# Kernel tuning notes

Hardware: AMD Instinct MI355X
Metric: run time of the kernel (lower is better)

Reference implementation:

```python
import jax, jax.numpy as jnp
import numpy as np

H = 64  # hidden size (fixed by module)

def _gru_cell(x, h, Wih, Whh, bih, bhh):
    # PyTorch GRU cell: gates ordered (r, z, n)
    gi = x @ Wih.T + bih            # [B, 3H]
    gh = h @ Whh.T + bhh            # [B, 3H]
    ir, iz, inn = jnp.split(gi, 3, axis=-1)
    hr, hz, hn = jnp.split(gh, 3, axis=-1)
    r = jax.nn.sigmoid(ir + hr)
    z = jax.nn.sigmoid(iz + hz)
    n = jnp.tanh(inn + r * hn)
    return (1.0 - z) * n + z * h


def setup_inputs() -> dict:
    key = jax.random.key(0)
    ks = jax.random.split(key, 24)
    B, T, NI = 16384, 256, 6
    s = 1.0 / np.sqrt(H)  # torch default GRU init scale
    f32 = jnp.float32
    u = lambda k, shp: jax.random.uniform(k, shp, dtype=f32, minval=-s, maxval=s)
    inp = {
        "x": jax.random.normal(ks[0], (B, T, NI), dtype=f32),
        "target_len": 180,
        # encoder GRU, layer 0 (input size NI) and layer 1 (input size H)
        "e_Wih0": u(ks[1], (3 * H, NI)), "e_Whh0": u(ks[2], (3 * H, H)),
        "e_bih0": u(ks[3], (3 * H,)),    "e_bhh0": u(ks[4], (3 * H,)),
        "e_Wih1": u(ks[5], (3 * H, H)),  "e_Whh1": u(ks[6], (3 * H, H)),
        "e_bih1": u(ks[7], (3 * H,)),    "e_bhh1": u(ks[8], (3 * H,)),
        # decoder GRU, layer 0 (input size 1) and layer 1 (input size H)
        "d_Wih0": u(ks[9], (3 * H, 1)),  "d_Whh0": u(ks[10], (3 * H, H)),
        "d_bih0": u(ks[11], (3 * H,)),   "d_bhh0": u(ks[12], (3 * H,)),
        "d_Wih1": u(ks[13], (3 * H, H)), "d_Whh1": u(ks[14], (3 * H, H)),
        "d_bih1": u(ks[15], (3 * H,)),   "d_bhh1": u(ks[16], (3 * H,)),
        # heads
        "W_on": u(ks[17], (1, H)), "b_on": u(ks[18], (1,)),
        "W_cv": u(ks[19], (1, H)), "b_cv": u(ks[20], (1,)),
    }
    return inp


def reference(x, target_len,
              e_Wih0, e_Whh0, e_bih0, e_bhh0, e_Wih1, e_Whh1, e_bih1, e_bhh1,
              d_Wih0, d_Whh0, d_bih0, d_bhh0, d_Wih1, d_Whh1, d_bih1, d_bhh1,
              W_on, b_on, W_cv, b_cv):
    B = x.shape[0]
    on_threshold = 0.5

    # ---- encoder: 2-layer GRU over the input sequence, keep final hidden ----
    def enc_step(carry, xt):
        h0, h1 = carry
        h0 = _gru_cell(xt, h0, e_Wih0, e_Whh0, e_bih0, e_bhh0)
        h1 = _gru_cell(h0, h1, e_Wih1, e_Whh1, e_bih1, e_bhh1)
        return (h0, h1), None

    h_init = (jnp.zeros((B, H), x.dtype), jnp.zeros((B, H), x.dtype))
    (h0, h1), _ = jax.lax.scan(enc_step, h_init, jnp.swapaxes(x, 0, 1))  # [T,B,NI]

    def dec_step(carry, _):
        prev, h0, h1 = carry                                   # prev: [B,1]
        h0 = _gru_cell(prev, h0, d_Wih0, d_Whh0, d_bih0, d_bhh0)
        h1 = _gru_cell(h0, h1, d_Wih1, d_Whh1, d_bih1, d_bhh1)
        cv = h1 @ W_cv.T + b_cv                                # [B,1]
        logit = h1 @ W_on.T + b_on                             # [B,1]
        gated = (jax.nn.sigmoid(logit) > on_threshold).astype(cv.dtype) * cv
        return (gated, h0, h1), gated

    prev0 = jnp.zeros((B, 1), x.dtype)
    _, outs = jax.lax.scan(dec_step, (prev0, h0, h1), None, length=target_len)
    # outs: [target_len, B, 1] -> [B, target_len, 1] (torch.cat along dim=1)
    return jnp.swapaxes(outs, 0, 1)
```

## Files before the change

### kernel.cpp

```cpp
#include <hip/hip_runtime.h>
#include <math.h>

#define TENC 256
#define NIE  6
#define LH   68
#define WSTR 68

__shared__ float sW1[192 * WSTR];
__shared__ float sU1[192 * WSTR];
__shared__ float sHd[132];
__shared__ float shs[3][64 * LH];

__device__ __forceinline__ float sigm_(float x) {
    return __builtin_amdgcn_rcpf(1.0f + __expf(-x));
}
__device__ __forceinline__ float tanh_(float x) {
    float t = __expf(2.0f * x);
    return (t - 1.0f) * __builtin_amdgcn_rcpf(t + 1.0f);
}

__device__ __forceinline__ void fma4(float& acc, const float4& a, const float4& b) {
    acc = fmaf(a.x, b.x, acc);
    acc = fmaf(a.y, b.y, acc);
    acc = fmaf(a.z, b.z, acc);
    acc = fmaf(a.w, b.w, acc);
}

__device__ __forceinline__ void stage_w1(const float* __restrict__ W1,
                                         const float* __restrict__ U1) {
    for (int s = threadIdx.x; s < 12288; s += 512) {
        int k = s & 63, row = s >> 6;
        int g = row >> 6, j = row & 63;
        int d = (j * 3 + g) * WSTR + k;
        sW1[d] = W1[s];
        sU1[d] = U1[s];
    }
}

template<int KIN>
__device__ __forceinline__ void layer0_c(const float* __restrict__ U0,
                                         const float* w0r, const float* w0z,
                                         const float* w0n,
                                         const float* xin,
                                         const float* b_r, const float* b_z,
                                         const float* b_nx, const float* b_nh,
                                         int jB, int bl,
                                         const float* __restrict__ hb,
                                         float hn[2][4])
{
    float ar[2][4], az[2][4], anx[2][4], anh[2][4];
#pragma unroll
    for (int g = 0; g < 4; ++g) {
#pragma unroll
        for (int jj = 0; jj < 2; ++jj) {
            ar[jj][g] = b_r[jj]; az[jj][g] = b_z[jj];
            anx[jj][g] = b_nx[jj]; anh[jj][g] = b_nh[jj];
        }
    }
#pragma unroll
    for (int jj = 0; jj < 2; ++jj)
#pragma unroll
        for (int g = 0; g < 4; ++g)
#pragma unroll
            for (int k = 0; k < KIN; ++k) {
                ar[jj][g]  = fmaf(w0r[jj * KIN + k], xin[g * KIN + k], ar[jj][g]);
                az[jj][g]  = fmaf(w0z[jj * KIN + k], xin[g * KIN + k], az[jj][g]);
                anx[jj][g] = fmaf(w0n[jj * KIN + k], xin[g * KIN + k], anx[jj][g]);
            }
    const float* u0 = U0 + (size_t)jB * 64;
    const float* u1 = U0 + (size_t)(jB + 1) * 64;
    const float* hr0 = hb + bl * LH;
#pragma unroll 2
    for (int kc = 0; kc < 64; kc += 4) {
        float4 hv[4];
#pragma unroll
        for (int g = 0; g < 4; ++g)
            hv[g] = *(const float4*)(hr0 + g * (16 * LH) + kc);
        float4 r0 = *(const float4*)(u0 + kc);
        float4 z0 = *(const float4*)(u0 + 4096 + kc);
        float4 n0 = *(const float4*)(u0 + 8192 + kc);
        float4 r1 = *(const float4*)(u1 + kc);
        float4 z1 = *(const float4*)(u1 + 4096 + kc);
        float4 n1 = *(const float4*)(u1 + 8192 + kc);
#pragma unroll
        for (int g = 0; g < 4; ++g) {
            fma4(ar[0][g], r0, hv[g]); fma4(az[0][g], z0, hv[g]); fma4(anh[0][g], n0, hv[g]);
            fma4(ar[1][g], r1, hv[g]); fma4(az[1][g], z1, hv[g]); fma4(anh[1][g], n1, hv[g]);
        }
    }
#pragma unroll
    for (int g = 0; g < 4; ++g) {
        float2 ho = *(const float2*)(hb + (bl + 16 * g) * LH + jB);
        float hold[2] = {ho.x, ho.y};
#pragma unroll
        for (int jj = 0; jj < 2; ++jj) {
            float r = sigm_(ar[jj][g]);
            float z = sigm_(az[jj][g]);
            float n = tanh_(fmaf(r, anh[jj][g], anx[jj][g]));
            hn[jj][g] = fmaf(z, hold[jj] - n, n);
        }
    }
}

__device__ __forceinline__ void layer1_c(const float* b_r, const float* b_z,
                                         const float* b_nx, const float* b_nh,
                                         int jB, int bl,
                                         const float* __restrict__ xb,
                                         const float* __restrict__ hb,
                                         float hn[2][4])
{
    float ar[2][4], az[2][4], anx[2][4], anh[2][4];
#pragma unroll
    for (int g = 0; g < 4; ++g) {
#pragma unroll
        for (int jj = 0; jj < 2; ++jj) {
            ar[jj][g] = b_r[jj]; az[jj][g] = b_z[jj];
            anx[jj][g] = b_nx[jj]; anh[jj][g] = b_nh[jj];
        }
    }
    const float* wb0 = sW1 + (jB * 3) * WSTR;
    const float* wb1 = sW1 + ((jB + 1) * 3) * WSTR;
    const float* ub0 = sU1 + (jB * 3) * WSTR;
    const float* ub1 = sU1 + ((jB + 1) * 3) * WSTR;
    const float* xr0 = xb + bl * LH;
    const float* hr0 = hb + bl * LH;
#pragma unroll 2
    for (int kc = 0; kc < 64; kc += 4) {
        float4 xv[4], hv[4];
#pragma unroll
        for (int g = 0; g < 4; ++g) {
            xv[g] = *(const float4*)(xr0 + g * (16 * LH) + kc);
            hv[g] = *(const float4*)(hr0 + g * (16 * LH) + kc);
        }
        float4 wr0 = *(const float4*)(wb0 + kc);
        float4 wz0 = *(const float4*)(wb0 + WSTR + kc);
        float4 wn0 = *(const float4*)(wb0 + 2 * WSTR + kc);
        float4 ur0 = *(const float4*)(ub0 + kc);
        float4 uz0 = *(const float4*)(ub0 + WSTR + kc);
        float4 un0 = *(const float4*)(ub0 + 2 * WSTR + kc);
        float4 wr1 = *(const float4*)(wb1 + kc);
        float4 wz1 = *(const float4*)(wb1 + WSTR + kc);
        float4 wn1 = *(const float4*)(wb1 + 2 * WSTR + kc);
        float4 ur1 = *(const float4*)(ub1 + kc);
        float4 uz1 = *(const float4*)(ub1 + WSTR + kc);
        float4 un1 = *(const float4*)(ub1 + 2 * WSTR + kc);
#pragma unroll
        for (int g = 0; g < 4; ++g) {
            fma4(ar[0][g], wr0, xv[g]);  fma4(ar[0][g], ur0, hv[g]);
            fma4(az[0][g], wz0, xv[g]);  fma4(az[0][g], uz0, hv[g]);
            fma4(anx[0][g], wn0, xv[g]); fma4(anh[0][g], un0, hv[g]);
            fma4(ar[1][g], wr1, xv[g]);  fma4(ar[1][g], ur1, hv[g]);
            fma4(az[1][g], wz1, xv[g]);  fma4(az[1][g], uz1, hv[g]);
            fma4(anx[1][g], wn1, xv[g]); fma4(anh[1][g], un1, hv[g]);
        }
    }
#pragma unroll
    for (int g = 0; g < 4; ++g) {
        float2 ho = *(const float2*)(hb + (bl + 16 * g) * LH + jB);
        float hold[2] = {ho.x, ho.y};
#pragma unroll
        for (int jj = 0; jj < 2; ++jj) {
            float r = sigm_(ar[jj][g]);
            float z = sigm_(az[jj][g]);
            float n = tanh_(fmaf(r, anh[jj][g], anx[jj][g]));
            hn[jj][g] = fmaf(z, hold[jj] - n, n);
        }
    }
}

extern "C" __global__ void __launch_bounds__(512, 2)
ccseq_kernel(const float* __restrict__ x, const int* __restrict__ p_tlen,
             const float* __restrict__ eW0, const float* __restrict__ eU0,
             const float* __restrict__ eBi0, const float* __restrict__ eBh0,
             const float* __restrict__ eW1, const float* __restrict__ eU1,
             const float* __restrict__ eBi1, const float* __restrict__ eBh1,
             const float* __restrict__ dW0, const float* __restrict__ dU0,
             const float* __restrict__ dBi0, const float* __restrict__ dBh0,
             const float* __restrict__ dW1, const float* __restrict__ dU1,
             const float* __restrict__ dBi1, const float* __restrict__ dBh1,
             const float* __restrict__ Won, const float* __restrict__ bon,
             const float* __restrict__ Wcv, const float* __restrict__ bcv,
             float* __restrict__ out)
{
    const int tid  = threadIdx.x;
    const int lane = tid & 63;
    const int wv   = tid >> 6;
    const int jg   = lane >> 4;
    const int bl   = lane & 15;
    const int jB   = wv * 8 + jg * 2;
    const int tlen = p_tlen[0];

    if (tid < 64) { sHd[tid] = Wcv[tid]; sHd[64 + tid] = Won[tid]; }
    for (int i = tid; i < 64 * LH; i += 512) {
        shs[0][i] = 0.0f; shs[1][i] = 0.0f; shs[2][i] = 0.0f;
    }
    stage_w1(eW1, eU1);
    __syncthreads();

    float w0r[2 * NIE], w0z[2 * NIE], w0n[2 * NIE];
#pragma unroll
    for (int jj = 0; jj < 2; ++jj)
#pragma unroll
        for (int k = 0; k < NIE; ++k) {
            w0r[jj * NIE + k] = eW0[(jB + jj) * NIE + k];
            w0z[jj * NIE + k] = eW0[(64 + jB + jj) * NIE + k];
            w0n[jj * NIE + k] = eW0[(128 + jB + jj) * NIE + k];
        }
    float eb_r[2], eb_z[2], eb_nx[2], eb_nh[2];
    float e1_r[2], e1_z[2], e1_nx[2], e1_nh[2];
#pragma unroll
    for (int jj = 0; jj < 2; ++jj) {
        int j = jB + jj;
        eb_r[jj]  = eBi0[j] + eBh0[j];
        eb_z[jj]  = eBi0[64 + j] + eBh0[64 + j];
        eb_nx[jj] = eBi0[128 + j];
        eb_nh[jj] = eBh0[128 + j];
        e1_r[jj]  = eBi1[j] + eBh1[j];
        e1_z[jj]  = eBi1[64 + j] + eBh1[64 + j];
        e1_nx[jj] = eBi1[128 + j];
        e1_nh[jj] = eBh1[128 + j];
    }

    const size_t bstr = (size_t)TENC * NIE;
    const float* xb[4];
#pragma unroll
    for (int g = 0; g < 4; ++g)
        xb[g] = x + (size_t)(blockIdx.x * 64 + bl + 16 * g) * bstr;

    float xc[4 * NIE];
    float hn[2][4], hn0[2][4];
#pragma unroll
    for (int g = 0; g < 4; ++g)
#pragma unroll
        for (int k = 0; k < NIE; ++k) xc[g * NIE + k] = xb[g][k];

    layer0_c<NIE>(eU0, w0r, w0z, w0n, xc, eb_r, eb_z, eb_nx, eb_nh,
                  jB, bl, shs[0] , hn0);
#pragma unroll
    for (int g = 0; g < 4; ++g)
        *(float2*)(shs[1] + (bl + 16 * g) * LH + jB) = make_float2(hn0[0][g], hn0[1][g]);
    __syncthreads();
    int ih0 = 1, ih1 = 2, ifr = 0;

    for (int t = 0; t < TENC; ++t) {
        if (t + 1 < TENC) {
#pragma unroll
            for (int g = 0; g < 4; ++g)
#pragma unroll
                for (int k = 0; k < NIE; ++k)
                    xc[g * NIE + k] = xb[g][(t + 1) * NIE + k];
        }

        layer1_c(e1_r, e1_z, e1_nx, e1_nh, jB, bl, shs[ih0], shs[ih1], hn);

        __builtin_amdgcn_sched_barrier(0);

        if (t + 1 < TENC) {
            layer0_c<NIE>(eU0, w0r, w0z, w0n, xc, eb_r, eb_z, eb_nx, eb_nh,
                          jB, bl, shs[ih0], hn0);
#pragma unroll
            for (int g = 0; g < 4; ++g)
                *(float2*)(shs[ifr] + (bl + 16 * g) * LH + jB) =
                    make_float2(hn0[0][g], hn0[1][g]);
        }
        __syncthreads();
#pragma unroll
        for (int g = 0; g < 4; ++g)
            *(float2*)(shs[ih1] + (bl + 16 * g) * LH + jB) =
                make_float2(hn[0][g], hn[1][g]);
        __syncthreads();

        if (t + 1 < TENC) { int o = ih0; ih0 = ifr; ifr = o; }
    }

    stage_w1(dW1, dU1);
    float v0r[2], v0z[2], v0n[2];
    float db_r[2], db_z[2], db_nx[2], db_nh[2];
    float d1_r[2], d1_z[2], d1_nx[2], d1_nh[2];
#pragma unroll
    for (int jj = 0; jj < 2; ++jj) {
        int j = jB + jj;
        v0r[jj] = dW0[j]; v0z[jj] = dW0[64 + j]; v0n[jj] = dW0[128 + j];
        db_r[jj]  = dBi0[j] + dBh0[j];
        db_z[jj]  = dBi0[64 + j] + dBh0[64 + j];
        db_nx[jj] = dBi0[128 + j];
        db_nh[jj] = dBh0[128 + j];
        d1_r[jj]  = dBi1[j] + dBh1[j];
        d1_z[jj]  = dBi1[64 + j] + dBh1[64 + j];
        d1_nx[jj] = dBi1[128 + j];
        d1_nh[jj] = dBh1[128 + j];
    }
    const float hbc = bcv[0], hbo = bon[0];
    __syncthreads();

    float prev[4] = {0.0f, 0.0f, 0.0f, 0.0f};
    for (int t = 0; t < tlen; ++t) {
        layer0_c<1>(dU0, v0r, v0z, v0n, prev, db_r, db_z, db_nx, db_nh,
                    jB, bl, shs[ih0], hn);
#pragma unroll
        for (int g = 0; g < 4; ++g)
            *(float2*)(shs[ifr] + (bl + 16 * g) * LH + jB) =
                make_float2(hn[0][g], hn[1][g]);
        __syncthreads();

        layer1_c(d1_r, d1_z, d1_nx, d1_nh, jB, bl, shs[ifr], shs[ih1], hn);
#pragma unroll
        for (int g = 0; g < 4; ++g)
            *(float2*)(shs[ih0] + (bl + 16 * g) * LH + jB) =
                make_float2(hn[0][g], hn[1][g]);
        __syncthreads();

        float cv[4] = {hbc, hbc, hbc, hbc};
        float lg[4] = {hbo, hbo, hbo, hbo};
        const float* hr0 = shs[ih0] + bl * LH;
#pragma unroll 2
        for (int kc = 0; kc < 64; kc += 4) {
            float4 wc = *(const float4*)(sHd + kc);
            float4 wo = *(const float4*)(sHd + 64 + kc);
#pragma unroll
            for (int g = 0; g < 4; ++g) {
                float4 h4 = *(const float4*)(hr0 + g * (16 * LH) + kc);
                fma4(cv[g], wc, h4);
                fma4(lg[g], wo, h4);
            }
        }
#pragma unroll
        for (int g = 0; g < 4; ++g)
            prev[g] = (lg[g] > 0.0f) ? cv[g] : 0.0f;
        if (tid < 16) {
#pragma unroll
            for (int g = 0; g < 4; ++g)
                out[(size_t)(blockIdx.x * 64 + bl + 16 * g) * tlen + t] = prev[g];
        }
        int o0 = ih0, o1 = ih1;
        ih0 = ifr; ih1 = o0; ifr = o1;
    }
}

extern "C" void kernel_launch(void* const* d_in, const int* in_sizes, int n_in,
                              void* d_out, int out_size, void* d_ws, size_t ws_size,
                              hipStream_t stream)
{
    (void)n_in; (void)out_size; (void)d_ws; (void)ws_size;
    const float* x    = (const float*)d_in[0];
    const int*   tl   = (const int*)d_in[1];
    const float* eW0  = (const float*)d_in[2];
    const float* eU0  = (const float*)d_in[3];
    const float* eBi0 = (const float*)d_in[4];
    const float* eBh0 = (const float*)d_in[5];
    const float* eW1  = (const float*)d_in[6];
    const float* eU1  = (const float*)d_in[7];
    const float* eBi1 = (const float*)d_in[8];
    const float* eBh1 = (const float*)d_in[9];
    const float* dW0  = (const float*)d_in[10];
    const float* dU0  = (const float*)d_in[11];
    const float* dBi0 = (const float*)d_in[12];
    const float* dBh0 = (const float*)d_in[13];
    const float* dW1  = (const float*)d_in[14];
    const float* dU1  = (const float*)d_in[15];
    const float* dBi1 = (const float*)d_in[16];
    const float* dBh1 = (const float*)d_in[17];
    const float* Won  = (const float*)d_in[18];
    const float* bon  = (const float*)d_in[19];
    const float* Wcv  = (const float*)d_in[20];
    const float* bcv  = (const float*)d_in[21];

    const int B    = in_sizes[0] / (TENC * NIE);
    const int nblk = B / 64;

    ccseq_kernel<<<dim3(nblk), dim3(512), 0, stream>>>(
        x, tl, eW0, eU0, eBi0, eBh0, eW1, eU1, eBi1, eBh1,
        dW0, dU0, dBi0, dBh0, dW1, dU1, dBi1, dBh1,
        Won, bon, Wcv, bcv, (float*)d_out);
}
```

Baseline: 8.472 ms.

## Use 1024-thread blocks with one hidden unit per thread

Each thread now computes one hidden unit instead of two, and the block size doubles from 512 to 1024 threads (16 waves). Since LDS use limits each CU to a single block, the aim is to double the resident waves so LDS and transcendental latency is better hidden in the serial recurrence. The cost is less register reuse of each loaded hidden-state vector, so LDS reads per FMA roughly double. Per-thread state, bias setup and shared-memory stores are rewritten to scalar form.

```diff
diff --git a/kernel.cpp b/kernel.cpp
--- a/kernel.cpp
+++ b/kernel.cpp
@@ -28,7 +28,7 @@
 
 __device__ __forceinline__ void stage_w1(const float* __restrict__ W1,
                                          const float* __restrict__ U1) {
-    for (int s = threadIdx.x; s < 12288; s += 512) {
+    for (int s = threadIdx.x; s < 12288; s += 1024) {
         int k = s & 63, row = s >> 6;
         int g = row >> 6, j = row & 63;
         int d = (j * 3 + g) * WSTR + k;
@@ -42,33 +42,26 @@
                                          const float* w0r, const float* w0z,
                                          const float* w0n,
                                          const float* xin,
-                                         const float* b_r, const float* b_z,
-                                         const float* b_nx, const float* b_nh,
-                                         int jB, int bl,
+                                         float b_r, float b_z,
+                                         float b_nx, float b_nh,
+                                         int j, int bl,
                                          const float* __restrict__ hb,
-                                         float hn[2][4])
+                                         float hn[4])
 {
-    float ar[2][4], az[2][4], anx[2][4], anh[2][4];
+    float ar[4], az[4], anx[4], anh[4];
 #pragma unroll
     for (int g = 0; g < 4; ++g) {
-#pragma unroll
-        for (int jj = 0; jj < 2; ++jj) {
-            ar[jj][g] = b_r[jj]; az[jj][g] = b_z[jj];
-            anx[jj][g] = b_nx[jj]; anh[jj][g] = b_nh[jj];
-        }
-    }
-#pragma unroll
-    for (int jj = 0; jj < 2; ++jj)
-#pragma unroll
-        for (int g = 0; g < 4; ++g)
-#pragma unroll
-            for (int k = 0; k < KIN; ++k) {
-                ar[jj][g]  = fmaf(w0r[jj * KIN + k], xin[g * KIN + k], ar[jj][g]);
-                az[jj][g]  = fmaf(w0z[jj * KIN + k], xin[g * KIN + k], az[jj][g]);
-                anx[jj][g] = fmaf(w0n[jj * KIN + k], xin[g * KIN + k], anx[jj][g]);
-            }
-    const float* u0 = U0 + (size_t)jB * 64;
-    const float* u1 = U0 + (size_t)(jB + 1) * 64;
+        ar[g] = b_r; az[g] = b_z; anx[g] = b_nx; anh[g] = b_nh;
+    }
+#pragma unroll
+    for (int g = 0; g < 4; ++g)
+#pragma unroll
+        for (int k = 0; k < KIN; ++k) {
+            ar[g]  = fmaf(w0r[k], xin[g * KIN + k], ar[g]);
+            az[g]  = fmaf(w0z[k], xin[g * KIN + k], az[g]);
+            anx[g] = fmaf(w0n[k], xin[g * KIN + k], anx[g]);
+        }
+    const float* u0 = U0 + (size_t)j * 64;
     const float* hr0 = hb + bl * LH;
 #pragma unroll 2
     for (int kc = 0; kc < 64; kc += 4) {
@@ -79,49 +72,35 @@
         float4 r0 = *(const float4*)(u0 + kc);
         float4 z0 = *(const float4*)(u0 + 4096 + kc);
         float4 n0 = *(const float4*)(u0 + 8192 + kc);
-        float4 r1 = *(const float4*)(u1 + kc);
-        float4 z1 = *(const float4*)(u1 + 4096 + kc);
-        float4 n1 = *(const float4*)(u1 + 8192 + kc);
 #pragma unroll
         for (int g = 0; g < 4; ++g) {
-            fma4(ar[0][g], r0, hv[g]); fma4(az[0][g], z0, hv[g]); fma4(anh[0][g], n0, hv[g]);
-            fma4(ar[1][g], r1, hv[g]); fma4(az[1][g], z1, hv[g]); fma4(anh[1][g], n1, hv[g]);
+            fma4(ar[g], r0, hv[g]); fma4(az[g], z0, hv[g]); fma4(anh[g], n0, hv[g]);
         }
     }
 #pragma unroll
     for (int g = 0; g < 4; ++g) {
-        float2 ho = *(const float2*)(hb + (bl + 16 * g) * LH + jB);
-        float hold[2] = {ho.x, ho.y};
-#pragma unroll
-        for (int jj = 0; jj < 2; ++jj) {
-            float r = sigm_(ar[jj][g]);
-            float z = sigm_(az[jj][g]);
-            float n = tanh_(fmaf(r, anh[jj][g], anx[jj][g]));
-            hn[jj][g] = fmaf(z, hold[jj] - n, n);
-        }
-    }
-}
-
-__device__ __forceinline__ void layer1_c(const float* b_r, const float* b_z,
-                                         const float* b_nx, const float* b_nh,
-                                         int jB, int bl,
+        float hold = hb[(bl + 16 * g) * LH + j];
+        float r = sigm_(ar[g]);
+        float z = sigm_(az[g]);
+        float n = tanh_(fmaf(r, anh[g], anx[g]));
+        hn[g] = fmaf(z, hold - n, n);
+    }
+}
+
+__device__ __forceinline__ void layer1_c(float b_r, float b_z,
+                                         float b_nx, float b_nh,
+                                         int j, int bl,
                                          const float* __restrict__ xb,
                                          const float* __restrict__ hb,
-                                         float hn[2][4])
+                                         float hn[4])
 {
-    float ar[2][4], az[2][4], anx[2][4], anh[2][4];
+    float ar[4], az[4], anx[4], anh[4];
 #pragma unroll
     for (int g = 0; g < 4; ++g) {
-#pragma unroll
-        for (int jj = 0; jj < 2; ++jj) {
-            ar[jj][g] = b_r[jj]; az[jj][g] = b_z[jj];
-            anx[jj][g] = b_nx[jj]; anh[jj][g] = b_nh[jj];
-        }
-    }
-    const float* wb0 = sW1 + (jB * 3) * WSTR;
-    const float* wb1 = sW1 + ((jB + 1) * 3) * WSTR;
-    const float* ub0 = sU1 + (jB * 3) * WSTR;
-    const float* ub1 = sU1 + ((jB + 1) * 3) * WSTR;
+        ar[g] = b_r; az[g] = b_z; anx[g] = b_nx; anh[g] = b_nh;
+    }
+    const float* wb = sW1 + (j * 3) * WSTR;
+    const float* ub = sU1 + (j * 3) * WSTR;
     const float* xr0 = xb + bl * LH;
     const float* hr0 = hb + bl * LH;
 #pragma unroll 2
@@ -132,43 +111,30 @@
             xv[g] = *(const float4*)(xr0 + g * (16 * LH) + kc);
             hv[g] = *(const float4*)(hr0 + g * (16 * LH) + kc);
         }
-        float4 wr0 = *(const float4*)(wb0 + kc);
-        float4 wz0 = *(const float4*)(wb0 + WSTR + kc);
-        float4 wn0 = *(const float4*)(wb0 + 2 * WSTR + kc);
-        float4 ur0 = *(const float4*)(ub0 + kc);
-        float4 uz0 = *(const float4*)(ub0 + WSTR + kc);
-        float4 un0 = *(const float4*)(ub0 + 2 * WSTR + kc);
-        float4 wr1 = *(const float4*)(wb1 + kc);
-        float4 wz1 = *(const float4*)(wb1 + WSTR + kc);
-        float4 wn1 = *(const float4*)(wb1 + 2 * WSTR + kc);
-        float4 ur1 = *(const float4*)(ub1 + kc);
-        float4 uz1 = *(const float4*)(ub1 + WSTR + kc);
-        float4 un1 = *(const float4*)(ub1 + 2 * WSTR + kc);
+        float4 wr = *(const float4*)(wb + kc);
+        float4 wz = *(const float4*)(wb + WSTR + kc);
+        float4 wn = *(const float4*)(wb + 2 * WSTR + kc);
+        float4 ur = *(const float4*)(ub + kc);
+        float4 uz = *(const float4*)(ub + WSTR + kc);
+        float4 un = *(const float4*)(ub + 2 * WSTR + kc);
 #pragma unroll
         for (int g = 0; g < 4; ++g) {
-            fma4(ar[0][g], wr0, xv[g]);  fma4(ar[0][g], ur0, hv[g]);
-            fma4(az[0][g], wz0, xv[g]);  fma4(az[0][g], uz0, hv[g]);
-            fma4(anx[0][g], wn0, xv[g]); fma4(anh[0][g], un0, hv[g]);
-            fma4(ar[1][g], wr1, xv[g]);  fma4(ar[1][g], ur1, hv[g]);
-            fma4(az[1][g], wz1, xv[g]);  fma4(az[1][g], uz1, hv[g]);
-            fma4(anx[1][g], wn1, xv[g]); fma4(anh[1][g], un1, hv[g]);
+            fma4(ar[g], wr, xv[g]);  fma4(ar[g], ur, hv[g]);
+            fma4(az[g], wz, xv[g]);  fma4(az[g], uz, hv[g]);
+            fma4(anx[g], wn, xv[g]); fma4(anh[g], un, hv[g]);
         }
     }
 #pragma unroll
     for (int g = 0; g < 4; ++g) {
-        float2 ho = *(const float2*)(hb + (bl + 16 * g) * LH + jB);
-        float hold[2] = {ho.x, ho.y};
-#pragma unroll
-        for (int jj = 0; jj < 2; ++jj) {
-            float r = sigm_(ar[jj][g]);
-            float z = sigm_(az[jj][g]);
-            float n = tanh_(fmaf(r, anh[jj][g], anx[jj][g]));
-            hn[jj][g] = fmaf(z, hold[jj] - n, n);
-        }
-    }
-}
-
-extern "C" __global__ void __launch_bounds__(512, 2)
+        float hold = hb[(bl + 16 * g) * LH + j];
+        float r = sigm_(ar[g]);
+        float z = sigm_(az[g]);
+        float n = tanh_(fmaf(r, anh[g], anx[g]));
+        hn[g] = fmaf(z, hold - n, n);
+    }
+}
+
+extern "C" __global__ void __launch_bounds__(1024)
 ccseq_kernel(const float* __restrict__ x, const int* __restrict__ p_tlen,
              const float* __restrict__ eW0, const float* __restrict__ eU0,
              const float* __restrict__ eBi0, const float* __restrict__ eBh0,
@@ -187,39 +153,31 @@
     const int wv   = tid >> 6;
     const int jg   = lane >> 4;
     const int bl   = lane & 15;
-    const int jB   = wv * 8 + jg * 2;
+    const int j    = wv * 4 + jg;
     const int tlen = p_tlen[0];
 
     if (tid < 64) { sHd[tid] = Wcv[tid]; sHd[64 + tid] = Won[tid]; }
-    for (int i = tid; i < 64 * LH; i += 512) {
+    for (int i = tid; i < 64 * LH; i += 1024) {
         shs[0][i] = 0.0f; shs[1][i] = 0.0f; shs[2][i] = 0.0f;
     }
     stage_w1(eW1, eU1);
     __syncthreads();
 
-    float w0r[2 * NIE], w0z[2 * NIE], w0n[2 * NIE];
-#pragma unroll
-    for (int jj = 0; jj < 2; ++jj)
-#pragma unroll
-        for (int k = 0; k < NIE; ++k) {
-            w0r[jj * NIE + k] = eW0[(jB + jj) * NIE + k];
-            w0z[jj * NIE + k] = eW0[(64 + jB + jj) * NIE + k];
-            w0n[jj * NIE + k] = eW0[(128 + jB + jj) * NIE + k];
-        }
-    float eb_r[2], eb_z[2], eb_nx[2], eb_nh[2];
-    float e1_r[2], e1_z[2], e1_nx[2], e1_nh[2];
-#pragma unroll
-    for (int jj = 0; jj < 2; ++jj) {
-        int j = jB + jj;
-        eb_r[jj]  = eBi0[j] + eBh0[j];
-        eb_z[jj]  = eBi0[64 + j] + eBh0[64 + j];
-        eb_nx[jj] = eBi0[128 + j];
-        eb_nh[jj] = eBh0[128 + j];
-        e1_r[jj]  = eBi1[j] + eBh1[j];
-        e1_z[jj]  = eBi1[64 + j] + eBh1[64 + j];
-        e1_nx[jj] = eBi1[128 + j];
-        e1_nh[jj] = eBh1[128 + j];
-    }
+    float w0r[NIE], w0z[NIE], w0n[NIE];
+#pragma unroll
+    for (int k = 0; k < NIE; ++k) {
+        w0r[k] = eW0[j * NIE + k];
+        w0z[k] = eW0[(64 + j) * NIE + k];
+        w0n[k] = eW0[(128 + j) * NIE + k];
+    }
+    const float eb_r  = eBi0[j] + eBh0[j];
+    const float eb_z  = eBi0[64 + j] + eBh0[64 + j];
+    const float eb_nx = eBi0[128 + j];
+    const float eb_nh = eBh0[128 + j];
+    const float e1_r  = eBi1[j] + eBh1[j];
+    const float e1_z  = eBi1[64 + j] + eBh1[64 + j];
+    const float e1_nx = eBi1[128 + j];
+    const float e1_nh = eBh1[128 + j];
 
     const size_t bstr = (size_t)TENC * NIE;
     const float* xb[4];
@@ -228,17 +186,17 @@
         xb[g] = x + (size_t)(blockIdx.x * 64 + bl + 16 * g) * bstr;
 
     float xc[4 * NIE];
-    float hn[2][4], hn0[2][4];
+    float hn[4], hn0[4];
 #pragma unroll
     for (int g = 0; g < 4; ++g)
 #pragma unroll
         for (int k = 0; k < NIE; ++k) xc[g * NIE + k] = xb[g][k];
 
     layer0_c<NIE>(eU0, w0r, w0z, w0n, xc, eb_r, eb_z, eb_nx, eb_nh,
-                  jB, bl, shs[0] , hn0);
+                  j, bl, shs[0] , hn0);
 #pragma unroll
     for (int g = 0; g < 4; ++g)
-        *(float2*)(shs[1] + (bl + 16 * g) * LH + jB) = make_float2(hn0[0][g], hn0[1][g]);
+        shs[1][(bl + 16 * g) * LH + j] = hn0[g];
     __syncthreads();
     int ih0 = 1, ih1 = 2, ifr = 0;
 
@@ -251,63 +209,52 @@
                     xc[g * NIE + k] = xb[g][(t + 1) * NIE + k];
         }
 
-        layer1_c(e1_r, e1_z, e1_nx, e1_nh, jB, bl, shs[ih0], shs[ih1], hn);
+        layer1_c(e1_r, e1_z, e1_nx, e1_nh, j, bl, shs[ih0], shs[ih1], hn);
 
         __builtin_amdgcn_sched_barrier(0);
 
         if (t + 1 < TENC) {
             layer0_c<NIE>(eU0, w0r, w0z, w0n, xc, eb_r, eb_z, eb_nx, eb_nh,
-                          jB, bl, shs[ih0], hn0);
+                          j, bl, shs[ih0], hn0);
 #pragma unroll
             for (int g = 0; g < 4; ++g)
-                *(float2*)(shs[ifr] + (bl + 16 * g) * LH + jB) =
-                    make_float2(hn0[0][g], hn0[1][g]);
+                shs[ifr][(bl + 16 * g) * LH + j] = hn0[g];
         }
         __syncthreads();
 #pragma unroll
         for (int g = 0; g < 4; ++g)
-            *(float2*)(shs[ih1] + (bl + 16 * g) * LH + jB) =
-                make_float2(hn[0][g], hn[1][g]);
+            shs[ih1][(bl + 16 * g) * LH + j] = hn[g];
         __syncthreads();
 
         if (t + 1 < TENC) { int o = ih0; ih0 = ifr; ifr = o; }
     }
 
     stage_w1(dW1, dU1);
-    float v0r[2], v0z[2], v0n[2];
-    float db_r[2], db_z[2], db_nx[2], db_nh[2];
-    float d1_r[2], d1_z[2], d1_nx[2], d1_nh[2];
-#pragma unroll
-    for (int jj = 0; jj < 2; ++jj) {
-        int j = jB + jj;
-        v0r[jj] = dW0[j]; v0z[jj] = dW0[64 + j]; v0n[jj] = dW0[128 + j];
-        db_r[jj]  = dBi0[j] + dBh0[j];
-        db_z[jj]  = dBi0[64 + j] + dBh0[64 + j];
-        db_nx[jj] = dBi0[128 + j];
-        db_nh[jj] = dBh0[128 + j];
-        d1_r[jj]  = dBi1[j] + dBh1[j];
-        d1_z[jj]  = dBi1[64 + j] + dBh1[64 + j];
-        d1_nx[jj] = dBi1[128 + j];
-        d1_nh[jj] = dBh1[128 + j];
-    }
+    const float v0r = dW0[j], v0z = dW0[64 + j], v0n = dW0[128 + j];
+    const float db_r  = dBi0[j] + dBh0[j];
+    const float db_z  = dBi0[64 + j] + dBh0[64 + j];
+    const float db_nx = dBi0[128 + j];
+    const float db_nh = dBh0[128 + j];
+    const float d1_r  = dBi1[j] + dBh1[j];
+    const float d1_z  = dBi1[64 + j] + dBh1[64 + j];
+    const float d1_nx = dBi1[128 + j];
+    const float d1_nh = dBh1[128 + j];
     const float hbc = bcv[0], hbo = bon[0];
     __syncthreads();
 
     float prev[4] = {0.0f, 0.0f, 0.0f, 0.0f};
     for (int t = 0; t < tlen; ++t) {
-        layer0_c<1>(dU0, v0r, v0z, v0n, prev, db_r, db_z, db_nx, db_nh,
-                    jB, bl, shs[ih0], hn);
-#pragma unroll
-        for (int g = 0; g < 4; ++g)
-            *(float2*)(shs[ifr] + (bl + 16 * g) * LH + jB) =
-                make_float2(hn[0][g], hn[1][g]);
+        layer0_c<1>(dU0, &v0r, &v0z, &v0n, prev, db_r, db_z, db_nx, db_nh,
+                    j, bl, shs[ih0], hn);
+#pragma unroll
+        for (int g = 0; g < 4; ++g)
+            shs[ifr][(bl + 16 * g) * LH + j] = hn[g];
         __syncthreads();
 
-        layer1_c(d1_r, d1_z, d1_nx, d1_nh, jB, bl, shs[ifr], shs[ih1], hn);
-#pragma unroll
-        for (int g = 0; g < 4; ++g)
-            *(float2*)(shs[ih0] + (bl + 16 * g) * LH + jB) =
-                make_float2(hn[0][g], hn[1][g]);
+        layer1_c(d1_r, d1_z, d1_nx, d1_nh, j, bl, shs[ifr], shs[ih1], hn);
+#pragma unroll
+        for (int g = 0; g < 4; ++g)
+            shs[ih0][(bl + 16 * g) * LH + j] = hn[g];
         __syncthreads();
 
         float cv[4] = {hbc, hbc, hbc, hbc};
@@ -368,7 +315,7 @@
     const int B    = in_sizes[0] / (TENC * NIE);
     const int nblk = B / 64;
 
-    ccseq_kernel<<<dim3(nblk), dim3(512), 0, stream>>>(
+    ccseq_kernel<<<dim3(nblk), dim3(1024), 0, stream>>>(
         x, tl, eW0, eU0, eBi0, eBh0, eW1, eU1, eBi1, eBh1,
         dW0, dU0, dBi0, dBh0, dW1, dU1, dBi1, dBh1,
         Won, bon, Wcv, bcv, (float*)d_out);
```

Result: slower. 10.58 ms (+24.9%).
